# Performance work log

Measured on AMD Instinct MI355X. Metric: run time of the kernel, lower is better.

The kernel has to match this reference:

```python
import jax, jax.numpy as jnp
import numpy as np

B, L, H, O = 2048, 256, 512, 1  # batch, input_len, hidden_size, output_size
EPS = 1e-5

def setup_inputs() -> dict:
    key = jax.random.key(0)
    ks = jax.random.split(key, 16)
    s = 0.05
    return {
        "x": jax.random.normal(ks[0], (B, 1, O), jnp.float32),
        "hidden": jax.random.normal(ks[1], (1, B, H), jnp.float32),
        "encoder_outputs": jax.random.normal(ks[2], (B, L, H), jnp.float32),
        # weights stored [in, out] (transposed torch Linear convention)
        "emb_W": jax.random.normal(ks[3], (O, H), jnp.float32) * s,
        "emb_b": jax.random.normal(ks[4], (H,), jnp.float32) * s,
        "attn_W": jax.random.normal(ks[5], (2 * H, L), jnp.float32) * s,
        "attn_b": jax.random.normal(ks[6], (L,), jnp.float32) * s,
        "comb_W": jax.random.normal(ks[7], (2 * H, H), jnp.float32) * s,
        "comb_b": jax.random.normal(ks[8], (H,), jnp.float32) * s,
        "gru_Wih": jax.random.normal(ks[9], (H, 3 * H), jnp.float32) * s,
        "gru_Whh": jax.random.normal(ks[10], (H, 3 * H), jnp.float32) * s,
        "gru_bih": jax.random.normal(ks[11], (3 * H,), jnp.float32) * s,
        "gru_bhh": jax.random.normal(ks[12], (3 * H,), jnp.float32) * s,
        "out_W": jax.random.normal(ks[13], (H, O), jnp.float32) * s,
        "out_b": jax.random.normal(ks[14], (O,), jnp.float32) * s,
    }

def reference(x, hidden, encoder_outputs, emb_W, emb_b, attn_W, attn_b,
              comb_W, comb_b, gru_Wih, gru_Whh, gru_bih, gru_bhh, out_W, out_b):
    # embedding + InstanceNorm1d over hidden dim (C=1 channel, length=H), no affine
    embedded = x @ emb_W + emb_b                      # [B,1,H]
    mu = jnp.mean(embedded, axis=-1, keepdims=True)
    var = jnp.var(embedded, axis=-1, keepdims=True)   # biased var, matches torch
    embedded = (embedded - mu) * jax.lax.rsqrt(var + EPS)
    # dropout = identity (inference)
    h_b = jnp.transpose(hidden, (1, 0, 2))            # [B,1,H]
    attn_logits = jnp.concatenate([embedded, h_b], axis=2) @ attn_W + attn_b  # [B,1,L]
    attn_weights = jax.nn.softmax(attn_logits, axis=2)
    attn_applied = jnp.einsum('bql,bld->bqd', attn_weights, encoder_outputs)  # [B,1,H]
    out = jnp.concatenate([embedded, attn_applied], axis=2) @ comb_W + comb_b
    out = jax.nn.relu(out)                            # [B,1,H]
    # single GRU step (num_layers=1, seq_len=1)
    xt = out[:, 0, :]                                 # [B,H]
    h0 = hidden[0]                                    # [B,H]
    gi = xt @ gru_Wih + gru_bih                       # [B,3H]
    gh = h0 @ gru_Whh + gru_bhh
    i_r, i_z, i_n = jnp.split(gi, 3, axis=-1)
    h_r, h_z, h_n = jnp.split(gh, 3, axis=-1)
    r = jax.nn.sigmoid(i_r + h_r)
    z = jax.nn.sigmoid(i_z + h_z)
    n = jnp.tanh(i_n + r * h_n)
    h_new = (1.0 - z) * n + z * h0                    # [B,H]
    output = h_new[:, None, :] @ out_W + out_b        # [B,1,O]
    return output, h_new[None, :, :], attn_weights
```

## Files before the change

kernel.cpp:

```cpp
#include <hip/hip_runtime.h>
#include <math.h>

#define NB 2048
#define NL 256
#define NH 512

typedef unsigned short ushort_t;
typedef unsigned int uint_t;
typedef short s16x8 __attribute__((ext_vector_type(8)));
typedef short s16x4 __attribute__((ext_vector_type(4)));
typedef float f32x4 __attribute__((ext_vector_type(4)));

__device__ __forceinline__ float wsum(float v){
  #pragma unroll
  for (int o = 32; o; o >>= 1) v += __shfl_xor(v, o);
  return v;
}
__device__ __forceinline__ float wmax(float v){
  #pragma unroll
  for (int o = 32; o; o >>= 1) v = fmaxf(v, __shfl_xor(v, o));
  return v;
}
__device__ __forceinline__ ushort_t f2bf(float f){
  union { float f; unsigned u; } v; v.f = f;
  unsigned r = v.u + 0x7fffu + ((v.u >> 16) & 1u);
  return (ushort_t)(r >> 16);
}

__global__ __launch_bounds__(256)
void kTiny(const float* __restrict__ eW, const float* __restrict__ eb,
           const float* __restrict__ attn_W,
           ushort_t* __restrict__ WTA, float* __restrict__ stats,
           float* __restrict__ p, float* __restrict__ q)
{
  const int bid = blockIdx.x, tid = threadIdx.x;
  if (bid < 32) {
    const int bx = bid & 3, by = bid >> 2;
    const int c = bx*64 + (tid & 63);
    const int ksub = by*64 + (tid >> 6)*16;
    ushort_t vals[16];
    #pragma unroll
    for (int kk = 0; kk < 16; ++kk)
      vals[kk] = f2bf(attn_W[(size_t)(512 + ksub + kk)*NL + c]);
    *(s16x8*)&WTA[(size_t)c*512 + ksub]     = *(s16x8*)&vals[0];
    *(s16x8*)&WTA[(size_t)c*512 + ksub + 8] = *(s16x8*)&vals[8];
    return;
  }
  {
    __shared__ float rw[4], rb[4];
    __shared__ float pa[4][64], pb[4][64];
    const int lane = tid & 63, wv = tid >> 6;
    float swv = eW[tid] + eW[tid + 256];
    float sbv = eb[tid] + eb[tid + 256];
    swv = wsum(swv); sbv = wsum(sbv);
    if (lane == 0) { rw[wv] = swv; rb[wv] = sbv; }
    __syncthreads();
    const float mW = (rw[0]+rw[1]+rw[2]+rw[3]) * (1.f/NH);
    const float mb = (rb[0]+rb[1]+rb[2]+rb[3]) * (1.f/NH);

    if (bid == 36) {
      float u0 = eW[tid]-mW, u1 = eW[tid+256]-mW;
      float v0 = eb[tid]-mb, v1 = eb[tid+256]-mb;
      float s2 = u0*u0 + u1*u1, s3 = u0*v0 + u1*v1, s4 = v0*v0 + v1*v1;
      s2 = wsum(s2); s3 = wsum(s3); s4 = wsum(s4);
      if (lane == 0) { pa[0][wv] = s2; pa[1][wv] = s3; pa[2][wv] = s4; }
      __syncthreads();
      if (tid == 0) {
        stats[0] = mW; stats[1] = mb;
        stats[2] = pa[0][0]+pa[0][1]+pa[0][2]+pa[0][3];
        stats[3] = pa[1][0]+pa[1][1]+pa[1][2]+pa[1][3];
        stats[4] = pa[2][0]+pa[2][1]+pa[2][2]+pa[2][3];
      }
      return;
    }
    const int c = (bid - 32)*64 + lane;
    const int hc = tid >> 6;
    float ap = 0.f, aq = 0.f;
    #pragma unroll 4
    for (int h = hc*128; h < hc*128 + 128; ++h) {
      float w = attn_W[(size_t)h*NL + c];
      ap = fmaf(eW[h]-mW, w, ap);
      aq = fmaf(eb[h]-mb, w, aq);
    }
    pa[hc][lane] = ap; pb[hc][lane] = aq;
    __syncthreads();
    if (hc == 0) {
      p[c] = pa[0][lane]+pa[1][lane]+pa[2][lane]+pa[3][lane];
      q[c] = pb[0][lane]+pb[1][lane]+pb[2][lane]+pb[3][lane];
    }
  }
}

__global__ __launch_bounds__(256)
void kLogits(const float* __restrict__ hidden, const ushort_t* __restrict__ WTA,
             const float* __restrict__ x, const float* __restrict__ stats,
             const float* __restrict__ p, const float* __restrict__ q,
             const float* __restrict__ attn_b, float* __restrict__ logits)
{
  __shared__ ushort_t As[128][72];
  __shared__ ushort_t Bs[64][72];
  const int tid = threadIdx.x, lane = tid & 63, wr = tid >> 6;
  const int m0 = blockIdx.x * 128, n0 = blockIdx.y * 64;

  f32x4 acc[2][4];
  #pragma unroll
  for (int i = 0; i < 2; ++i)
    #pragma unroll
    for (int j = 0; j < 4; ++j)
      acc[i][j] = (f32x4){0.f,0.f,0.f,0.f};

  const int srow = tid >> 3, scol = (tid & 7) * 8;
  for (int kt = 0; kt < 512; kt += 64) {
    __syncthreads();
    #pragma unroll
    for (int it = 0; it < 4; ++it) {
      const int r = srow + it*32;
      const float* hp = hidden + (size_t)(m0+r)*NH + kt + scol;
      float4 v0 = *(const float4*)hp;
      float4 v1 = *(const float4*)(hp + 4);
      s16x8 o;
      o[0]=f2bf(v0.x); o[1]=f2bf(v0.y); o[2]=f2bf(v0.z); o[3]=f2bf(v0.w);
      o[4]=f2bf(v1.x); o[5]=f2bf(v1.y); o[6]=f2bf(v1.z); o[7]=f2bf(v1.w);
      *(s16x8*)&As[r][scol] = o;
    }
    #pragma unroll
    for (int it = 0; it < 2; ++it) {
      const int r = srow + it*32;
      *(s16x8*)&Bs[r][scol] = *(const s16x8*)&WTA[(size_t)(n0+r)*512 + kt + scol];
    }
    __syncthreads();
    #pragma unroll
    for (int ks = 0; ks < 2; ++ks) {
      const int ko = ks*32 + (lane >> 4)*8;
      s16x8 af[2], bfr[4];
      #pragma unroll
      for (int i = 0; i < 2; ++i) af[i]  = *(const s16x8*)&As[wr*32 + i*16 + (lane & 15)][ko];
      #pragma unroll
      for (int j = 0; j < 4; ++j) bfr[j] = *(const s16x8*)&Bs[j*16 + (lane & 15)][ko];
      #pragma unroll
      for (int i = 0; i < 2; ++i)
        #pragma unroll
        for (int j = 0; j < 4; ++j)
          acc[i][j] = __builtin_amdgcn_mfma_f32_16x16x32_bf16(af[i], bfr[j], acc[i][j], 0, 0, 0);
    }
  }

  const float S2 = stats[2], S3 = stats[3], S4 = stats[4];
  #pragma unroll
  for (int i = 0; i < 2; ++i) {
    #pragma unroll
    for (int reg = 0; reg < 4; ++reg) {
      const int row = m0 + wr*32 + i*16 + ((lane >> 4) << 2) + reg;
      const float xv = x[row];
      const float rs = rsqrtf((xv*xv*S2 + 2.f*xv*S3 + S4)*(1.0f/NH) + 1e-5f);
      const float al = xv*rs, be = rs;
      #pragma unroll
      for (int j = 0; j < 4; ++j) {
        const int col = n0 + j*16 + (lane & 15);
        logits[(size_t)row*NL + col] = acc[i][j][reg] + attn_b[col] + al*p[col] + be*q[col];
      }
    }
  }
}

__global__ __launch_bounds__(256)
void kStreamMega(const float* __restrict__ hidden,
                 const float* __restrict__ Wih, const float* __restrict__ Whh,
                 const float* __restrict__ comb_W,
                 const float* __restrict__ eW, const float* __restrict__ eb,
                 const float* __restrict__ out_b,
                 const float* __restrict__ logits, const float* __restrict__ enc,
                 ushort_t* __restrict__ A2, ushort_t* __restrict__ WTG,
                 ushort_t* __restrict__ WTC,
                 float* __restrict__ p2, float* __restrict__ q2,
                 float* __restrict__ out0,
                 float* __restrict__ attn_out, ushort_t* __restrict__ ABF)
{
  const int bid = blockIdx.x, tid = threadIdx.x;
  if (bid < 2048) {
    __shared__ float wl[NL];
    __shared__ __align__(16) float4 ps[128];
    __shared__ float sred[4];
    const int lane = tid & 63, wv = tid >> 6;
    const int b = bid;

    float lg = logits[(size_t)b*NL + tid];
    float m = wmax(lg);
    if (lane == 0) sred[wv] = m;
    __syncthreads();
    m = fmaxf(fmaxf(sred[0], sred[1]), fmaxf(sred[2], sred[3]));
    float e = expf(lg - m);
    float s = wsum(e);
    __syncthreads();
    if (lane == 0) sred[wv] = s;
    __syncthreads();
    const float inv = 1.f / (sred[0] + sred[1] + sred[2] + sred[3]);
    e *= inv;
    wl[tid] = e;
    attn_out[(size_t)b*NL + tid] = e;
    __syncthreads();

    const int col = tid & 127, half = tid >> 7;
    const f32x4* ep = (const f32x4*)(enc + (size_t)b*NL*NH);
    float4 acc = {0.f,0.f,0.f,0.f};
    #pragma unroll 4
    for (int l = half*128; l < half*128 + 128; ++l) {
      float w = wl[l];
      f32x4 ev = __builtin_nontemporal_load(ep + l*(NH/4) + col);
      acc.x = fmaf(w,ev[0],acc.x); acc.y = fmaf(w,ev[1],acc.y);
      acc.z = fmaf(w,ev[2],acc.z); acc.w = fmaf(w,ev[3],acc.w);
    }
    if (half == 0) ps[col] = acc;
    __syncthreads();
    if (half == 1) {
      float4 o = ps[col];
      o.x += acc.x; o.y += acc.y; o.z += acc.z; o.w += acc.w;
      s16x4 ov; ov[0]=f2bf(o.x); ov[1]=f2bf(o.y); ov[2]=f2bf(o.z); ov[3]=f2bf(o.w);
      *(s16x4*)&ABF[(size_t)b*NH + col*4] = ov;
    }
    return;
  }
  if (bid < 2560) {
    const int idx = ((bid-2048)*256 + tid) * 8;
    const int b = idx >> 9, h = idx & 511;
    float4 v0 = *(const float4*)(hidden + idx);
    float4 v1 = *(const float4*)(hidden + idx + 4);
    s16x8 o;
    o[0]=f2bf(v0.x); o[1]=f2bf(v0.y); o[2]=f2bf(v0.z); o[3]=f2bf(v0.w);
    o[4]=f2bf(v1.x); o[5]=f2bf(v1.y); o[6]=f2bf(v1.z); o[7]=f2bf(v1.w);
    *(s16x8*)&A2[(size_t)b*1024 + 512 + h] = o;
    return;
  }
  if (bid < 3072) {
    const int b2 = bid - 2560, bx = b2 & 31, by = b2 >> 5;
    const int n = bx*64 + (tid & 63);
    const int ksub = by*64 + (tid >> 6)*16;
    const int g = n >> 6, t = (n >> 4) & 3, c = (g << 4) | (n & 15);
    const int sc = (t == 0) ? c : (t == 1) ? (512 + c) : (1024 + c);
    ushort_t vals[16];
    #pragma unroll
    for (int kk = 0; kk < 16; ++kk) {
      int k = ksub + kk;
      float v;
      if (k < 512) v = (t == 3) ? 0.f : Wih[(size_t)k*1536 + sc];
      else         v = (t == 2) ? 0.f : Whh[(size_t)(k-512)*1536 + sc];
      vals[kk] = f2bf(v);
    }
    *(s16x8*)&WTG[(size_t)n*1024 + ksub]     = *(s16x8*)&vals[0];
    *(s16x8*)&WTG[(size_t)n*1024 + ksub + 8] = *(s16x8*)&vals[8];
    return;
  }
  if (bid < 3136) {
    const int b2 = bid - 3072, bx = b2 & 7, by = b2 >> 3;
    const int c = bx*64 + (tid & 63);
    const int ksub = by*64 + (tid >> 6)*16;
    ushort_t vals[16];
    #pragma unroll
    for (int kk = 0; kk < 16; ++kk)
      vals[kk] = f2bf(comb_W[(size_t)(512 + ksub + kk)*NH + c]);
    *(s16x8*)&WTC[(size_t)c*512 + ksub]     = *(s16x8*)&vals[0];
    *(s16x8*)&WTC[(size_t)c*512 + ksub + 8] = *(s16x8*)&vals[8];
    return;
  }
  if (bid < 3144) {
    __shared__ float rw[4], rb[4];
    __shared__ float pa[4][64], pb[4][64];
    const int lane = tid & 63, wv = tid >> 6;
    float swv = eW[tid] + eW[tid + 256];
    float sbv = eb[tid] + eb[tid + 256];
    swv = wsum(swv); sbv = wsum(sbv);
    if (lane == 0) { rw[wv] = swv; rb[wv] = sbv; }
    __syncthreads();
    const float mW = (rw[0]+rw[1]+rw[2]+rw[3]) * (1.f/NH);
    const float mb = (rb[0]+rb[1]+rb[2]+rb[3]) * (1.f/NH);
    const int c = (bid - 3136)*64 + lane;
    const int hc = tid >> 6;
    float ap = 0.f, aq = 0.f;
    #pragma unroll 4
    for (int h = hc*128; h < hc*128 + 128; ++h) {
      float w = comb_W[(size_t)h*NH + c];
      ap = fmaf(eW[h]-mW, w, ap);
      aq = fmaf(eb[h]-mb, w, aq);
    }
    pa[hc][lane] = ap; pb[hc][lane] = aq;
    __syncthreads();
    if (hc == 0) {
      p2[c] = pa[0][lane]+pa[1][lane]+pa[2][lane]+pa[3][lane];
      q2[c] = pb[0][lane]+pb[1][lane]+pb[2][lane]+pb[3][lane];
    }
    return;
  }
  out0[(bid-3144)*256 + tid] = out_b[0];
}

__global__ __launch_bounds__(256)
void kComb(const ushort_t* __restrict__ ABF, const ushort_t* __restrict__ WTC,
           const float* __restrict__ x, const float* __restrict__ stats,
           const float* __restrict__ p2, const float* __restrict__ q2,
           const float* __restrict__ comb_b, ushort_t* __restrict__ A2)
{
  __shared__ ushort_t As[128][72];
  __shared__ ushort_t Bs[64][72];
  const int tid = threadIdx.x, lane = tid & 63, wr = tid >> 6;
  const int m0 = blockIdx.x * 128, n0 = blockIdx.y * 64;

  f32x4 acc[2][4];
  #pragma unroll
  for (int i = 0; i < 2; ++i)
    #pragma unroll
    for (int j = 0; j < 4; ++j)
      acc[i][j] = (f32x4){0.f,0.f,0.f,0.f};

  const int srow = tid >> 3, scol = (tid & 7) * 8;
  for (int kt = 0; kt < 512; kt += 64) {
    __syncthreads();
    #pragma unroll
    for (int it = 0; it < 4; ++it) {
      const int r = srow + it*32;
      *(s16x8*)&As[r][scol] = *(const s16x8*)&ABF[(size_t)(m0+r)*512 + kt + scol];
    }
    #pragma unroll
    for (int it = 0; it < 2; ++it) {
      const int r = srow + it*32;
      *(s16x8*)&Bs[r][scol] = *(const s16x8*)&WTC[(size_t)(n0+r)*512 + kt + scol];
    }
    __syncthreads();
    #pragma unroll
    for (int ks = 0; ks < 2; ++ks) {
      const int ko = ks*32 + (lane >> 4)*8;
      s16x8 af[2], bfr[4];
      #pragma unroll
      for (int i = 0; i < 2; ++i) af[i]  = *(const s16x8*)&As[wr*32 + i*16 + (lane & 15)][ko];
      #pragma unroll
      for (int j = 0; j < 4; ++j) bfr[j] = *(const s16x8*)&Bs[j*16 + (lane & 15)][ko];
      #pragma unroll
      for (int i = 0; i < 2; ++i)
        #pragma unroll
        for (int j = 0; j < 4; ++j)
          acc[i][j] = __builtin_amdgcn_mfma_f32_16x16x32_bf16(af[i], bfr[j], acc[i][j], 0, 0, 0);
    }
  }

  const float S2 = stats[2], S3 = stats[3], S4 = stats[4];
  #pragma unroll
  for (int i = 0; i < 2; ++i) {
    #pragma unroll
    for (int reg = 0; reg < 4; ++reg) {
      const int row = m0 + wr*32 + i*16 + ((lane >> 4) << 2) + reg;
      const float xv = x[row];
      const float rs = rsqrtf((xv*xv*S2 + 2.f*xv*S3 + S4)*(1.0f/NH) + 1e-5f);
      const float al = xv*rs, be = rs;
      #pragma unroll
      for (int j = 0; j < 4; ++j) {
        const int col = n0 + j*16 + (lane & 15);
        float v = acc[i][j][reg] + comb_b[col] + al*p2[col] + be*q2[col];
        A2[(size_t)row*1024 + col] = f2bf(fmaxf(v, 0.f));
      }
    }
  }
}

__global__ __launch_bounds__(256)
void kGRU(const ushort_t* __restrict__ A, const ushort_t* __restrict__ Bt,
          const float* __restrict__ bih, const float* __restrict__ bhh,
          const float* __restrict__ hidden, const float* __restrict__ out_W,
          float* __restrict__ h_out, float* __restrict__ out0)
{
  __shared__ ushort_t As[128][72];
  __shared__ ushort_t Bs[64][72];
  const int tid = threadIdx.x, lane = tid & 63, wr = tid >> 6;
  const int m0 = blockIdx.x * 128, n0 = blockIdx.y * 64;

  f32x4 acc[2][4];
  #pragma unroll
  for (int i = 0; i < 2; ++i)
    #pragma unroll
    for (int j = 0; j < 4; ++j)
      acc[i][j] = (f32x4){0.f,0.f,0.f,0.f};

  const int srow = tid >> 3, scol = (tid & 7) * 8;

  for (int kt = 0; kt < 512; kt += 64) {
    __syncthreads();
    #pragma unroll
    for (int it = 0; it < 4; ++it) {
      const int r = srow + it*32;
      *(s16x8*)&As[r][scol] = *(const s16x8*)&A[(size_t)(m0+r)*1024 + kt + scol];
    }
    {
      *(s16x8*)&Bs[srow][scol] = *(const s16x8*)&Bt[(size_t)(n0+srow)*1024 + kt + scol];
      if (srow < 16) {
        const int r = srow + 32;
        *(s16x8*)&Bs[r][scol] = *(const s16x8*)&Bt[(size_t)(n0+r)*1024 + kt + scol];
      }
    }
    __syncthreads();
    #pragma unroll
    for (int ks = 0; ks < 2; ++ks) {
      const int ko = ks*32 + (lane >> 4)*8;
      s16x8 af[2], b0, b1, b2;
      #pragma unroll
      for (int i = 0; i < 2; ++i) af[i] = *(const s16x8*)&As[wr*32 + i*16 + (lane & 15)][ko];
      b0 = *(const s16x8*)&Bs[0*16 + (lane & 15)][ko];
      b1 = *(const s16x8*)&Bs[1*16 + (lane & 15)][ko];
      b2 = *(const s16x8*)&Bs[2*16 + (lane & 15)][ko];
      #pragma unroll
      for (int i = 0; i < 2; ++i) {
        acc[i][0] = __builtin_amdgcn_mfma_f32_16x16x32_bf16(af[i], b0, acc[i][0], 0, 0, 0);
        acc[i][1] = __builtin_amdgcn_mfma_f32_16x16x32_bf16(af[i], b1, acc[i][1], 0, 0, 0);
        acc[i][2] = __builtin_amdgcn_mfma_f32_16x16x32_bf16(af[i], b2, acc[i][2], 0, 0, 0);
      }
    }
  }
  for (int kt = 512; kt < 1024; kt += 64) {
    __syncthreads();
    #pragma unroll
    for (int it = 0; it < 4; ++it) {
      const int r = srow + it*32;
      *(s16x8*)&As[r][scol] = *(const s16x8*)&A[(size_t)(m0+r)*1024 + kt + scol];
    }
    {
      *(s16x8*)&Bs[srow][scol] = *(const s16x8*)&Bt[(size_t)(n0+srow)*1024 + kt + scol];
      if (srow >= 16) {
        const int r = srow + 32;
        *(s16x8*)&Bs[r][scol] = *(const s16x8*)&Bt[(size_t)(n0+r)*1024 + kt + scol];
      }
    }
    __syncthreads();
    #pragma unroll
    for (int ks = 0; ks < 2; ++ks) {
      const int ko = ks*32 + (lane >> 4)*8;
      s16x8 af[2], b0, b1, b3;
      #pragma unroll
      for (int i = 0; i < 2; ++i) af[i] = *(const s16x8*)&As[wr*32 + i*16 + (lane & 15)][ko];
      b0 = *(const s16x8*)&Bs[0*16 + (lane & 15)][ko];
      b1 = *(const s16x8*)&Bs[1*16 + (lane & 15)][ko];
      b3 = *(const s16x8*)&Bs[3*16 + (lane & 15)][ko];
      #pragma unroll
      for (int i = 0; i < 2; ++i) {
        acc[i][0] = __builtin_amdgcn_mfma_f32_16x16x32_bf16(af[i], b0, acc[i][0], 0, 0, 0);
        acc[i][1] = __builtin_amdgcn_mfma_f32_16x16x32_bf16(af[i], b1, acc[i][1], 0, 0, 0);
        acc[i][3] = __builtin_amdgcn_mfma_f32_16x16x32_bf16(af[i], b3, acc[i][3], 0, 0, 0);
      }
    }
  }

  const int g = n0 >> 6;
  const int hcol = (g << 4) | (lane & 15);
  const float b_r = bih[hcol]        + bhh[hcol];
  const float b_z = bih[512 + hcol]  + bhh[512 + hcol];
  const float b_i = bih[1024 + hcol];
  const float b_h = bhh[1024 + hcol];
  const float ow  = out_W[hcol];
  #pragma unroll
  for (int i = 0; i < 2; ++i) {
    #pragma unroll
    for (int reg = 0; reg < 4; ++reg) {
      const int row = m0 + wr*32 + i*16 + ((lane >> 4) << 2) + reg;
      float rv = 1.f / (1.f + expf(-(acc[i][0][reg] + b_r)));
      float zv = 1.f / (1.f + expf(-(acc[i][1][reg] + b_z)));
      float nv = tanhf(acc[i][2][reg] + b_i + rv * (acc[i][3][reg] + b_h));
      float h0v = hidden[(size_t)row*NH + hcol];
      float hn = nv + zv * (h0v - nv);
      h_out[(size_t)row*NH + hcol] = hn;
      float partial = hn * ow;
      #pragma unroll
      for (int o = 1; o < 16; o <<= 1) partial += __shfl_xor(partial, o);
      if ((lane & 15) == 0) atomicAdd(&out0[row], partial);
    }
  }
}

extern "C" void kernel_launch(void* const* d_in, const int* in_sizes, int n_in,
                              void* d_out, int out_size, void* d_ws, size_t ws_size,
                              hipStream_t stream)
{
  const float* x      = (const float*)d_in[0];
  const float* hidden = (const float*)d_in[1];
  const float* enc    = (const float*)d_in[2];
  const float* emb_W  = (const float*)d_in[3];
  const float* emb_b  = (const float*)d_in[4];
  const float* attn_W = (const float*)d_in[5];
  const float* attn_b = (const float*)d_in[6];
  const float* comb_W = (const float*)d_in[7];
  const float* comb_b = (const float*)d_in[8];
  const float* Wih    = (const float*)d_in[9];
  const float* Whh    = (const float*)d_in[10];
  const float* bih    = (const float*)d_in[11];
  const float* bhh    = (const float*)d_in[12];
  const float* out_W  = (const float*)d_in[13];
  const float* out_b  = (const float*)d_in[14];

  float* out      = (float*)d_out;
  float* out0     = out;
  float* out_h    = out + NB;
  float* out_attn = out + NB + (size_t)NB*NH;

  float* wsf    = (float*)d_ws;
  float* stats  = wsf;
  float* p      = wsf + 16;
  float* q      = wsf + 272;
  float* p2     = wsf + 528;
  float* q2     = wsf + 1040;
  float* logits = wsf + 2048;
  ushort_t* usb = (ushort_t*)(wsf + 526400);
  ushort_t* A2  = usb;
  ushort_t* ABF = usb + 2097152;
  ushort_t* WTA = usb + 3145728;
  ushort_t* WTC = usb + 3276800;
  ushort_t* WTG = usb + 3538944;

  kTiny<<<37, 256, 0, stream>>>(emb_W, emb_b, attn_W, WTA, stats, p, q);
  kLogits<<<dim3(16, 4), 256, 0, stream>>>(hidden, WTA, x, stats, p, q,
                                           attn_b, logits);
  kStreamMega<<<3152, 256, 0, stream>>>(hidden, Wih, Whh, comb_W, emb_W, emb_b,
                                        out_b, logits, enc, A2, WTG, WTC,
                                        p2, q2, out0, out_attn, ABF);
  kComb<<<dim3(16, 8), 256, 0, stream>>>(ABF, WTC, x, stats, p2, q2, comb_b, A2);
  kGRU<<<dim3(16, 32), 256, 0, stream>>>(A2, WTG, bih, bhh, hidden, out_W,
                                         out_h, out0);
}
```

Baseline: 246.2 us.

## Fuse comb GEMM into streaming mega-kernel via per-row-tile atomic counters

Moves the comb_W bf16 transpose and p2/q2 precompute into the small prologue kernel, then folds the comb GEMM into the streaming kernel. The GEMM blocks spin on global atomic counters until all 128 attention rows of their M-tile have written ABF. This removes one kernel launch and lets the comb GEMM overlap with the tail of the encoder streaming. The cost is reliance on block scheduling order: the spinning GEMM blocks have the highest block indices and wait on lower ones, which could deadlock if dispatch order were not guaranteed. They also occupy CUs while they spin.

```diff
diff --git a/kernel.cpp b/kernel.cpp
--- a/kernel.cpp
+++ b/kernel.cpp
@@ -6,7 +6,6 @@
 #define NH 512
 
 typedef unsigned short ushort_t;
-typedef unsigned int uint_t;
 typedef short s16x8 __attribute__((ext_vector_type(8)));
 typedef short s16x4 __attribute__((ext_vector_type(4)));
 typedef float f32x4 __attribute__((ext_vector_type(4)));
@@ -29,9 +28,12 @@
 
 __global__ __launch_bounds__(256)
 void kTiny(const float* __restrict__ eW, const float* __restrict__ eb,
-           const float* __restrict__ attn_W,
-           ushort_t* __restrict__ WTA, float* __restrict__ stats,
-           float* __restrict__ p, float* __restrict__ q)
+           const float* __restrict__ attn_W, const float* __restrict__ comb_W,
+           ushort_t* __restrict__ WTA, ushort_t* __restrict__ WTC,
+           float* __restrict__ stats,
+           float* __restrict__ p, float* __restrict__ q,
+           float* __restrict__ p2, float* __restrict__ q2,
+           int* __restrict__ ctr)
 {
   const int bid = blockIdx.x, tid = threadIdx.x;
   if (bid < 32) {
@@ -44,6 +46,18 @@
       vals[kk] = f2bf(attn_W[(size_t)(512 + ksub + kk)*NL + c]);
     *(s16x8*)&WTA[(size_t)c*512 + ksub]     = *(s16x8*)&vals[0];
     *(s16x8*)&WTA[(size_t)c*512 + ksub + 8] = *(s16x8*)&vals[8];
+    return;
+  }
+  if (bid < 96) {
+    const int b2 = bid - 32, bx = b2 & 7, by = b2 >> 3;
+    const int c = bx*64 + (tid & 63);
+    const int ksub = by*64 + (tid >> 6)*16;
+    ushort_t vals[16];
+    #pragma unroll
+    for (int kk = 0; kk < 16; ++kk)
+      vals[kk] = f2bf(comb_W[(size_t)(512 + ksub + kk)*NH + c]);
+    *(s16x8*)&WTC[(size_t)c*512 + ksub]     = *(s16x8*)&vals[0];
+    *(s16x8*)&WTC[(size_t)c*512 + ksub + 8] = *(s16x8*)&vals[8];
     return;
   }
   {
@@ -58,7 +72,8 @@
     const float mW = (rw[0]+rw[1]+rw[2]+rw[3]) * (1.f/NH);
     const float mb = (rb[0]+rb[1]+rb[2]+rb[3]) * (1.f/NH);
 
-    if (bid == 36) {
+    if (bid == 108) {
+      if (tid < 16) ctr[tid] = 0;
       float u0 = eW[tid]-mW, u1 = eW[tid+256]-mW;
       float v0 = eb[tid]-mb, v1 = eb[tid+256]-mb;
       float s2 = u0*u0 + u1*u1, s3 = u0*v0 + u1*v1, s4 = v0*v0 + v1*v1;
@@ -73,20 +88,24 @@
       }
       return;
     }
-    const int c = (bid - 32)*64 + lane;
+    const int bid2 = bid - 96;
+    const float* Wsrc; int ldw, c0; float *op, *oq;
+    if (bid2 < 4) { Wsrc = attn_W; ldw = NL; c0 = bid2*64;     op = p  + c0; oq = q  + c0; }
+    else          { Wsrc = comb_W; ldw = NH; c0 = (bid2-4)*64; op = p2 + c0; oq = q2 + c0; }
+    const int c = c0 + lane;
     const int hc = tid >> 6;
     float ap = 0.f, aq = 0.f;
     #pragma unroll 4
     for (int h = hc*128; h < hc*128 + 128; ++h) {
-      float w = attn_W[(size_t)h*NL + c];
+      float w = Wsrc[(size_t)h*ldw + c];
       ap = fmaf(eW[h]-mW, w, ap);
       aq = fmaf(eb[h]-mb, w, aq);
     }
     pa[hc][lane] = ap; pb[hc][lane] = aq;
     __syncthreads();
     if (hc == 0) {
-      p[c] = pa[0][lane]+pa[1][lane]+pa[2][lane]+pa[3][lane];
-      q[c] = pb[0][lane]+pb[1][lane]+pb[2][lane]+pb[3][lane];
+      op[lane] = pa[0][lane]+pa[1][lane]+pa[2][lane]+pa[3][lane];
+      oq[lane] = pb[0][lane]+pb[1][lane]+pb[2][lane]+pb[3][lane];
     }
   }
 }
@@ -164,17 +183,17 @@
 }
 
 __global__ __launch_bounds__(256)
-void kStreamMega(const float* __restrict__ hidden,
-                 const float* __restrict__ Wih, const float* __restrict__ Whh,
-                 const float* __restrict__ comb_W,
-                 const float* __restrict__ eW, const float* __restrict__ eb,
-                 const float* __restrict__ out_b,
-                 const float* __restrict__ logits, const float* __restrict__ enc,
-                 ushort_t* __restrict__ A2, ushort_t* __restrict__ WTG,
-                 ushort_t* __restrict__ WTC,
-                 float* __restrict__ p2, float* __restrict__ q2,
-                 float* __restrict__ out0,
-                 float* __restrict__ attn_out, ushort_t* __restrict__ ABF)
+void kMega(const float* __restrict__ hidden,
+           const float* __restrict__ Wih, const float* __restrict__ Whh,
+           const float* __restrict__ out_b,
+           const float* __restrict__ logits, const float* __restrict__ enc,
+           const ushort_t* __restrict__ WTC,
+           const float* __restrict__ x, const float* __restrict__ stats,
+           const float* __restrict__ p2, const float* __restrict__ q2,
+           const float* __restrict__ comb_b,
+           ushort_t* __restrict__ A2, ushort_t* __restrict__ WTG,
+           float* __restrict__ out0, int* __restrict__ ctr,
+           float* __restrict__ attn_out, ushort_t* __restrict__ ABF)
 {
   const int bid = blockIdx.x, tid = threadIdx.x;
   if (bid < 2048) {
@@ -217,6 +236,11 @@
       o.x += acc.x; o.y += acc.y; o.z += acc.z; o.w += acc.w;
       s16x4 ov; ov[0]=f2bf(o.x); ov[1]=f2bf(o.y); ov[2]=f2bf(o.z); ov[3]=f2bf(o.w);
       *(s16x4*)&ABF[(size_t)b*NH + col*4] = ov;
+    }
+    __syncthreads();
+    if (tid == 0) {
+      __threadfence();
+      atomicAdd(&ctr[b >> 7], 1);
     }
     return;
   }
@@ -250,111 +274,75 @@
     *(s16x8*)&WTG[(size_t)n*1024 + ksub + 8] = *(s16x8*)&vals[8];
     return;
   }
-  if (bid < 3136) {
-    const int b2 = bid - 3072, bx = b2 & 7, by = b2 >> 3;
-    const int c = bx*64 + (tid & 63);
-    const int ksub = by*64 + (tid >> 6)*16;
-    ushort_t vals[16];
-    #pragma unroll
-    for (int kk = 0; kk < 16; ++kk)
-      vals[kk] = f2bf(comb_W[(size_t)(512 + ksub + kk)*NH + c]);
-    *(s16x8*)&WTC[(size_t)c*512 + ksub]     = *(s16x8*)&vals[0];
-    *(s16x8*)&WTC[(size_t)c*512 + ksub + 8] = *(s16x8*)&vals[8];
+  if (bid < 3080) {
+    out0[(bid-3072)*256 + tid] = out_b[0];
     return;
   }
-  if (bid < 3144) {
-    __shared__ float rw[4], rb[4];
-    __shared__ float pa[4][64], pb[4][64];
-    const int lane = tid & 63, wv = tid >> 6;
-    float swv = eW[tid] + eW[tid + 256];
-    float sbv = eb[tid] + eb[tid + 256];
-    swv = wsum(swv); sbv = wsum(sbv);
-    if (lane == 0) { rw[wv] = swv; rb[wv] = sbv; }
-    __syncthreads();
-    const float mW = (rw[0]+rw[1]+rw[2]+rw[3]) * (1.f/NH);
-    const float mb = (rb[0]+rb[1]+rb[2]+rb[3]) * (1.f/NH);
-    const int c = (bid - 3136)*64 + lane;
-    const int hc = tid >> 6;
-    float ap = 0.f, aq = 0.f;
-    #pragma unroll 4
-    for (int h = hc*128; h < hc*128 + 128; ++h) {
-      float w = comb_W[(size_t)h*NH + c];
-      ap = fmaf(eW[h]-mW, w, ap);
-      aq = fmaf(eb[h]-mb, w, aq);
-    }
-    pa[hc][lane] = ap; pb[hc][lane] = aq;
-    __syncthreads();
-    if (hc == 0) {
-      p2[c] = pa[0][lane]+pa[1][lane]+pa[2][lane]+pa[3][lane];
-      q2[c] = pb[0][lane]+pb[1][lane]+pb[2][lane]+pb[3][lane];
-    }
-    return;
-  }
-  out0[(bid-3144)*256 + tid] = out_b[0];
-}
-
-__global__ __launch_bounds__(256)
-void kComb(const ushort_t* __restrict__ ABF, const ushort_t* __restrict__ WTC,
-           const float* __restrict__ x, const float* __restrict__ stats,
-           const float* __restrict__ p2, const float* __restrict__ q2,
-           const float* __restrict__ comb_b, ushort_t* __restrict__ A2)
-{
-  __shared__ ushort_t As[128][72];
-  __shared__ ushort_t Bs[64][72];
-  const int tid = threadIdx.x, lane = tid & 63, wr = tid >> 6;
-  const int m0 = blockIdx.x * 128, n0 = blockIdx.y * 64;
-
-  f32x4 acc[2][4];
-  #pragma unroll
-  for (int i = 0; i < 2; ++i)
-    #pragma unroll
-    for (int j = 0; j < 4; ++j)
-      acc[i][j] = (f32x4){0.f,0.f,0.f,0.f};
-
-  const int srow = tid >> 3, scol = (tid & 7) * 8;
-  for (int kt = 0; kt < 512; kt += 64) {
-    __syncthreads();
-    #pragma unroll
-    for (int it = 0; it < 4; ++it) {
-      const int r = srow + it*32;
-      *(s16x8*)&As[r][scol] = *(const s16x8*)&ABF[(size_t)(m0+r)*512 + kt + scol];
-    }
-    #pragma unroll
-    for (int it = 0; it < 2; ++it) {
-      const int r = srow + it*32;
-      *(s16x8*)&Bs[r][scol] = *(const s16x8*)&WTC[(size_t)(n0+r)*512 + kt + scol];
-    }
-    __syncthreads();
-    #pragma unroll
-    for (int ks = 0; ks < 2; ++ks) {
-      const int ko = ks*32 + (lane >> 4)*8;
-      s16x8 af[2], bfr[4];
-      #pragma unroll
-      for (int i = 0; i < 2; ++i) af[i]  = *(const s16x8*)&As[wr*32 + i*16 + (lane & 15)][ko];
-      #pragma unroll
-      for (int j = 0; j < 4; ++j) bfr[j] = *(const s16x8*)&Bs[j*16 + (lane & 15)][ko];
-      #pragma unroll
-      for (int i = 0; i < 2; ++i)
+  {
+    __shared__ ushort_t As[128][72];
+    __shared__ ushort_t Bs[64][72];
+    const int b2 = bid - 3080;
+    const int m0 = (b2 >> 3) * 128, n0 = (b2 & 7) * 64;
+    const int lane = tid & 63, wr = tid >> 6;
+
+    if (tid == 0) {
+      while (atomicAdd(&ctr[m0 >> 7], 0) < 128) __builtin_amdgcn_s_sleep(32);
+    }
+    __syncthreads();
+    __threadfence();
+
+    f32x4 acc[2][4];
+    #pragma unroll
+    for (int i = 0; i < 2; ++i)
+      #pragma unroll
+      for (int j = 0; j < 4; ++j)
+        acc[i][j] = (f32x4){0.f,0.f,0.f,0.f};
+
+    const int srow = tid >> 3, scol = (tid & 7) * 8;
+    for (int kt = 0; kt < 512; kt += 64) {
+      __syncthreads();
+      #pragma unroll
+      for (int it = 0; it < 4; ++it) {
+        const int r = srow + it*32;
+        *(s16x8*)&As[r][scol] = *(const s16x8*)&ABF[(size_t)(m0+r)*512 + kt + scol];
+      }
+      #pragma unroll
+      for (int it = 0; it < 2; ++it) {
+        const int r = srow + it*32;
+        *(s16x8*)&Bs[r][scol] = *(const s16x8*)&WTC[(size_t)(n0+r)*512 + kt + scol];
+      }
+      __syncthreads();
+      #pragma unroll
+      for (int ks = 0; ks < 2; ++ks) {
+        const int ko = ks*32 + (lane >> 4)*8;
+        s16x8 af[2], bfr[4];
         #pragma unroll
-        for (int j = 0; j < 4; ++j)
-          acc[i][j] = __builtin_amdgcn_mfma_f32_16x16x32_bf16(af[i], bfr[j], acc[i][j], 0, 0, 0);
-    }
-  }
-
-  const float S2 = stats[2], S3 = stats[3], S4 = stats[4];
-  #pragma unroll
-  for (int i = 0; i < 2; ++i) {
-    #pragma unroll
-    for (int reg = 0; reg < 4; ++reg) {
-      const int row = m0 + wr*32 + i*16 + ((lane >> 4) << 2) + reg;
-      const float xv = x[row];
-      const float rs = rsqrtf((xv*xv*S2 + 2.f*xv*S3 + S4)*(1.0f/NH) + 1e-5f);
-      const float al = xv*rs, be = rs;
-      #pragma unroll
-      for (int j = 0; j < 4; ++j) {
-        const int col = n0 + j*16 + (lane & 15);
-        float v = acc[i][j][reg] + comb_b[col] + al*p2[col] + be*q2[col];
-        A2[(size_t)row*1024 + col] = f2bf(fmaxf(v, 0.f));
+        for (int i = 0; i < 2; ++i) af[i]  = *(const s16x8*)&As[wr*32 + i*16 + (lane & 15)][ko];
+        #pragma unroll
+        for (int j = 0; j < 4; ++j) bfr[j] = *(const s16x8*)&Bs[j*16 + (lane & 15)][ko];
+        #pragma unroll
+        for (int i = 0; i < 2; ++i)
+          #pragma unroll
+          for (int j = 0; j < 4; ++j)
+            acc[i][j] = __builtin_amdgcn_mfma_f32_16x16x32_bf16(af[i], bfr[j], acc[i][j], 0, 0, 0);
+      }
+    }
+
+    const float S2 = stats[2], S3 = stats[3], S4 = stats[4];
+    #pragma unroll
+    for (int i = 0; i < 2; ++i) {
+      #pragma unroll
+      for (int reg = 0; reg < 4; ++reg) {
+        const int row = m0 + wr*32 + i*16 + ((lane >> 4) << 2) + reg;
+        const float xv = x[row];
+        const float rs = rsqrtf((xv*xv*S2 + 2.f*xv*S3 + S4)*(1.0f/NH) + 1e-5f);
+        const float al = xv*rs, be = rs;
+        #pragma unroll
+        for (int j = 0; j < 4; ++j) {
+          const int col = n0 + j*16 + (lane & 15);
+          float v = acc[i][j][reg] + comb_b[col] + al*p2[col] + be*q2[col];
+          A2[(size_t)row*1024 + col] = f2bf(fmaxf(v, 0.f));
+        }
       }
     }
   }
@@ -497,11 +485,12 @@
   float* out_attn = out + NB + (size_t)NB*NH;
 
   float* wsf    = (float*)d_ws;
-  float* stats  = wsf;
-  float* p      = wsf + 16;
-  float* q      = wsf + 272;
-  float* p2     = wsf + 528;
-  float* q2     = wsf + 1040;
+  int*   ctr    = (int*)wsf;
+  float* stats  = wsf + 16;
+  float* p      = wsf + 32;
+  float* q      = wsf + 288;
+  float* p2     = wsf + 544;
+  float* q2     = wsf + 1056;
   float* logits = wsf + 2048;
   ushort_t* usb = (ushort_t*)(wsf + 526400);
   ushort_t* A2  = usb;
@@ -510,13 +499,13 @@
   ushort_t* WTC = usb + 3276800;
   ushort_t* WTG = usb + 3538944;
 
-  kTiny<<<37, 256, 0, stream>>>(emb_W, emb_b, attn_W, WTA, stats, p, q);
+  kTiny<<<109, 256, 0, stream>>>(emb_W, emb_b, attn_W, comb_W,
+                                 WTA, WTC, stats, p, q, p2, q2, ctr);
   kLogits<<<dim3(16, 4), 256, 0, stream>>>(hidden, WTA, x, stats, p, q,
                                            attn_b, logits);
-  kStreamMega<<<3152, 256, 0, stream>>>(hidden, Wih, Whh, comb_W, emb_W, emb_b,
-                                        out_b, logits, enc, A2, WTG, WTC,
-                                        p2, q2, out0, out_attn, ABF);
-  kComb<<<dim3(16, 8), 256, 0, stream>>>(ABF, WTC, x, stats, p2, q2, comb_b, A2);
+  kMega<<<3208, 256, 0, stream>>>(hidden, Wih, Whh, out_b, logits, enc,
+                                  WTC, x, stats, p2, q2, comb_b,
+                                  A2, WTG, out0, ctr, out_attn, ABF);
   kGRU<<<dim3(16, 32), 256, 0, stream>>>(A2, WTG, bih, bhh, hidden, out_W,
                                          out_h, out0);
 }
```

After: 358.3 us. +45.5%, slower.
